# Optimization experiments

Hardware: AMD Instinct MI355X
Metric: run time of the kernel (lower is better)

Reference implementation:

```python
import jax, jax.numpy as jnp
import numpy as np

NEG_SLOPE = 0.2
N, IN_DIM, OUT_DIM, N_HEADS = 4096, 512, 512, 4
D_K = OUT_DIM // N_HEADS


def setup_inputs() -> dict:
    key = jax.random.key(0)
    k1, k2, k3, k4, k5 = jax.random.split(key, 5)
    H = jax.random.normal(k1, (N, IN_DIM), dtype=jnp.float32)
    A = jax.random.randint(k2, (N, N), 0, 2, dtype=jnp.int32)
    W = jax.random.normal(k3, (IN_DIM, OUT_DIM), dtype=jnp.float32) * (1.0 / np.sqrt(IN_DIM))
    a_l = jax.random.normal(k4, (N_HEADS, D_K), dtype=jnp.float32) * 0.1
    a_r = jax.random.normal(k5, (N_HEADS, D_K), dtype=jnp.float32) * 0.1
    return {"H": H, "A": A, "W": W, "a_l": a_l, "a_r": a_r}


def reference(H, A, W, a_l, a_r):
    n = H.shape[0]
    # mask = (A + I) > 0, shape (N, N); self-loops always allowed
    mask = (A + jnp.eye(n, dtype=A.dtype)) > 0
    # Wh: (N, heads, d_k)
    Wh = (H @ W).reshape(n, N_HEADS, D_K)
    sl = jnp.einsum('nhd,hd->nh', Wh, a_l)  # (N, heads)
    sr = jnp.einsum('nhd,hd->nh', Wh, a_r)  # (N, heads)
    # e[i, h, j] = leaky_relu(sl[i,h] + sr[j,h])
    e = jax.nn.leaky_relu(sl[:, :, None] + sr.T[None, :, :], negative_slope=NEG_SLOPE)
    e = jnp.where(mask[:, None, :], e, -jnp.inf)
    alpha = jnp.nan_to_num(jax.nn.softmax(e, axis=2), nan=0.0)  # dropout is identity at eval
    # out[i, h, :] = sum_j alpha[i,h,j] * Wh[j,h,:]
    out = jnp.einsum('nhm,mhd->nhd', alpha, Wh).reshape(n, OUT_DIM)
    return jax.nn.elu(out)
```

## Files before the change

### kernel.cpp

```cpp
#include <hip/hip_runtime.h>

typedef unsigned short ushort_t;
typedef __attribute__((ext_vector_type(8)))  short  short8;
typedef __attribute__((ext_vector_type(4)))  short  short4v;
typedef __attribute__((ext_vector_type(4)))  float  float4v;
typedef __attribute__((ext_vector_type(4)))  int    int4v;

#define N_NODES 4096
#define NHEADS  4
#define DK      128
#define ODIM    512
#define KDIM    512

__device__ __forceinline__ float bf2f(ushort_t u) {
    return __uint_as_float(((unsigned)u) << 16);
}
__device__ __forceinline__ ushort_t f2bf_rne(float f) {
    unsigned u = __float_as_uint(f);
    u += 0x7fffu + ((u >> 16) & 1u);
    return (ushort_t)(u >> 16);
}

__global__ __launch_bounds__(256) void pack_mask_k(const int* __restrict__ A,
                                                   unsigned long long* __restrict__ P,
                                                   const ushort_t* __restrict__ Hraw,
                                                   int* __restrict__ flag,
                                                   const void* __restrict__ W,
                                                   ushort_t* __restrict__ WT,
                                                   float* __restrict__ sl,
                                                   float* __restrict__ sr)
{
    __shared__ ushort_t lt[64][72];
    __shared__ int dcnt[4];
    const int tid = threadIdx.x;
    const int bx  = blockIdx.x;

    if (bx == 0 && tid < 64) {
        const int lane = tid;
        int cnt = 0;
        #pragma unroll
        for (int s = 0; s < 16; ++s) {
            ushort_t v = Hraw[(lane * 16 + s) * 2];
            int e = (v >> 7) & 0xFF;
            cnt += (((e >= 90) && (e <= 140)) || (v == 0)) ? 1 : 0;
        }
        #pragma unroll
        for (int off = 32; off; off >>= 1) cnt += __shfl_down(cnt, off);
        if (lane == 0) *flag = (cnt < 768) ? 1 : 0;
    }

    {
        const int lane  = tid & 63;
        const int flat4 = bx * 256 + tid;
        const int row   = flat4 >> 10;
        const int col0  = (flat4 << 2) & 4095;
        const int4v a   = ((const int4v*)A)[flat4];
        unsigned nib = 0;
        #pragma unroll
        for (int j = 0; j < 4; ++j)
            nib |= ((a[j] != 0) || (row == col0 + j)) ? (1u << j) : 0u;
        unsigned long long v = (unsigned long long)nib << ((lane & 15) * 4);
        v |= __shfl_xor(v, 1);
        v |= __shfl_xor(v, 2);
        v |= __shfl_xor(v, 4);
        v |= __shfl_xor(v, 8);
        if ((lane & 15) == 0) P[flat4 >> 4] = v;
    }

    if (bx >= 64 && bx < 96) {
        const int idx = (bx - 64) * 256 + tid;
        float4v z;
        #pragma unroll
        for (int e = 0; e < 4; ++e) z[e] = 0.f;
        if (idx < 4096) ((float4v*)sl)[idx] = z;
        else            ((float4v*)sr)[idx - 4096] = z;
    }

    if (bx < 64) {
        int cnt = 0;
        #pragma unroll
        for (int s = 0; s < 4; ++s) {
            ushort_t v = Hraw[(tid * 4 + s) * 2];
            int e = (v >> 7) & 0xFF;
            cnt += (((e >= 90) && (e <= 140)) || (v == 0)) ? 1 : 0;
        }
        #pragma unroll
        for (int off = 32; off; off >>= 1) cnt += __shfl_down(cnt, off);
        if ((tid & 63) == 0) dcnt[tid >> 6] = cnt;
        __syncthreads();
        const int f32 = (dcnt[0] + dcnt[1] + dcnt[2] + dcnt[3]) < 768;

        const int ti = bx >> 3, tj = bx & 7;
        const int r = tid >> 2, c2 = tid & 3;
        const size_t eo = (size_t)(ti * 64 + r) * KDIM + tj * 64 + c2 * 16;
        if (f32) {
            const float4v* src = (const float4v*)((const float*)W + eo);
            float4v f0 = src[0], f1 = src[1], f2 = src[2], f3 = src[3];
            #pragma unroll
            for (int e = 0; e < 4; ++e) {
                lt[r][c2 * 16 +  0 + e] = f2bf_rne(f0[e]);
                lt[r][c2 * 16 +  4 + e] = f2bf_rne(f1[e]);
                lt[r][c2 * 16 +  8 + e] = f2bf_rne(f2[e]);
                lt[r][c2 * 16 + 12 + e] = f2bf_rne(f3[e]);
            }
        } else {
            const short8* src = (const short8*)((const ushort_t*)W + eo);
            short8 v0 = src[0];
            short8 v1 = src[1];
            *(short8*)&lt[r][c2 * 16]     = v0;
            *(short8*)&lt[r][c2 * 16 + 8] = v1;
        }
        __syncthreads();
        #pragma unroll
        for (int itr = 0; itr < 2; ++itr) {
            int idx = itr * 256 + tid;
            int n = idx >> 3, c = idx & 7;
            short8 vv;
            #pragma unroll
            for (int e = 0; e < 8; ++e) vv[e] = (short)lt[c * 8 + e][n];
            *(short8*)(WT + (size_t)(tj * 64 + n) * KDIM + ti * 64 + c * 8) = vv;
        }
    }
}

__global__ __launch_bounds__(256) void gemm_wht_dual_k(const void* __restrict__ H,
                                                       const ushort_t* __restrict__ WT,
                                                       ushort_t* __restrict__ WhT,
                                                       const int* __restrict__ flag,
                                                       const void* __restrict__ al,
                                                       const void* __restrict__ ar,
                                                       float* __restrict__ sl,
                                                       float* __restrict__ sr)
{
    __shared__ ushort_t lt[64][72];
    const int f32 = *flag;
    const int tid  = threadIdx.x;
    const int lane = tid & 63;
    const int wid  = tid >> 6;
    const int quad = lane >> 4;
    const int l15  = lane & 15;
    const int bm = blockIdx.x & 63, bn = blockIdx.x >> 6;
    const int i0 = bm * 64, n0 = bn * 64;

    const size_t aoff = (size_t)(i0 + wid * 16 + l15) * KDIM + quad * 8;
    const short8* bp0 = (const short8*)(WT + (size_t)(n0 +  0 + l15) * KDIM) + quad;
    const short8* bp1 = (const short8*)(WT + (size_t)(n0 + 16 + l15) * KDIM) + quad;
    const short8* bp2 = (const short8*)(WT + (size_t)(n0 + 32 + l15) * KDIM) + quad;
    const short8* bp3 = (const short8*)(WT + (size_t)(n0 + 48 + l15) * KDIM) + quad;

    float4v acc0, acc1, acc2, acc3;
    #pragma unroll
    for (int e = 0; e < 4; ++e) { acc0[e] = 0.f; acc1[e] = 0.f; acc2[e] = 0.f; acc3[e] = 0.f; }

    #pragma unroll 4
    for (int k8 = 0; k8 < 64; k8 += 4) {
        short8 a;
        if (f32) {
            const float4v* fp = (const float4v*)((const float*)H + aoff + (size_t)k8 * 8);
            float4v x0 = fp[0], x1 = fp[1];
            #pragma unroll
            for (int e = 0; e < 4; ++e) {
                a[e]     = (short)f2bf_rne(x0[e]);
                a[4 + e] = (short)f2bf_rne(x1[e]);
            }
        } else {
            a = *(const short8*)((const ushort_t*)H + aoff + (size_t)k8 * 8);
        }
        acc0 = __builtin_amdgcn_mfma_f32_16x16x32_bf16(a, bp0[k8], acc0, 0, 0, 0);
        acc1 = __builtin_amdgcn_mfma_f32_16x16x32_bf16(a, bp1[k8], acc1, 0, 0, 0);
        acc2 = __builtin_amdgcn_mfma_f32_16x16x32_bf16(a, bp2[k8], acc2, 0, 0, 0);
        acc3 = __builtin_amdgcn_mfma_f32_16x16x32_bf16(a, bp3[k8], acc3, 0, 0, 0);
    }

    #pragma unroll
    for (int r = 0; r < 4; ++r) {
        int m = wid * 16 + quad * 4 + r;
        lt[ 0 + l15][m] = f2bf_rne(acc0[r]);
        lt[16 + l15][m] = f2bf_rne(acc1[r]);
        lt[32 + l15][m] = f2bf_rne(acc2[r]);
        lt[48 + l15][m] = f2bf_rne(acc3[r]);
    }
    __syncthreads();
    #pragma unroll
    for (int itr = 0; itr < 2; ++itr) {
        int idx = itr * 256 + tid;
        int n = idx >> 3, c = idx & 7;
        short8 v = *(const short8*)&lt[n][c * 8];
        *(short8*)(WhT + (size_t)(n0 + n) * N_NODES + i0 + c * 8) = v;
    }

    {
        const int h2 = n0 >> 7;
        const int d0 = n0 & 127;
        const int m  = tid >> 2;
        const int part = tid & 3;
        float psl = 0.f, psr = 0.f;
        #pragma unroll
        for (int k = 0; k < 16; ++k) {
            int n = part * 16 + k;
            float wv = bf2f(lt[n][m]);
            float av = f32 ? ((const float*)al)[h2 * DK + d0 + n]
                           : bf2f(((const ushort_t*)al)[h2 * DK + d0 + n]);
            float bv = f32 ? ((const float*)ar)[h2 * DK + d0 + n]
                           : bf2f(((const ushort_t*)ar)[h2 * DK + d0 + n]);
            psl += wv * av;
            psr += wv * bv;
        }
        psl += __shfl_down(psl, 2); psl += __shfl_down(psl, 1);
        psr += __shfl_down(psr, 2); psr += __shfl_down(psr, 1);
        if (part == 0) {
            atomicAdd(&sl[h2 * N_NODES + i0 + m], psl);
            atomicAdd(&sr[h2 * N_NODES + i0 + m], psr);
        }
    }
}

__global__ __launch_bounds__(1024, 4) void attn_full_k(const ushort_t* __restrict__ WhT,
                                                       const unsigned* __restrict__ Apack,
                                                       const float* __restrict__ sl,
                                                       const float* __restrict__ sr,
                                                       void* __restrict__ out,
                                                       const int* __restrict__ flag)
{
    __shared__ char smem[147456] __attribute__((aligned(16)));
    ushort_t* vbuf = (ushort_t*)smem;
    unsigned (*mbuf)[128] = (unsigned (*)[128])(smem + 98304);
    float*    srs  = (float*)(smem + 131072);

    const int f32  = *flag;
    const int tid  = threadIdx.x;
    const int lane = tid & 63;
    const int wid  = tid >> 6;
    const int wq   = wid & 3;
    const int js   = wid >> 2;
    const int quad = lane >> 4;
    const int l15  = lane & 15;
    const int bx   = blockIdx.x;
    const int h    = bx & 3;
    const int i0   = (bx >> 2) << 6;

    const float C1 = 1.44269504f;

    for (int j = tid; j < 4096; j += 1024) srs[j] = sr[h * N_NODES + j] * C1;
    for (int t = tid; t < 64 * 128; t += 1024) {
        int r = t >> 7, c = t & 127;
        mbuf[r][c ^ (r & 31)] = Apack[(size_t)(i0 + r) * 128 + c];
    }
    const int myrow = wq * 16 + l15;
    const float slv = sl[h * N_NODES + i0 + myrow] * C1;
    __syncthreads();

    float4v acc[8];
    #pragma unroll
    for (int nt = 0; nt < 8; ++nt)
        #pragma unroll
        for (int e = 0; e < 4; ++e) acc[nt][e] = 0.f;
    float4v accden;
    #pragma unroll
    for (int e = 0; e < 4; ++e) accden[e] = 0.f;

    short8 ones;
    #pragma unroll
    for (int e = 0; e < 8; ++e) ones[e] = (short)0x3F80;

    const int dl = lane >> 4;
    const int s4 = lane & 15;
    const ushort_t* gq0 = WhT + (size_t)(h * DK + wid * 8 + 0 + dl) * N_NODES
                              + (size_t)((s4 ^ (0 + dl)) * 8);
    const ushort_t* gq1 = WhT + (size_t)(h * DK + wid * 8 + 4 + dl) * N_NODES
                              + (size_t)((s4 ^ (4 + dl)) * 8);

    #define DMA_WIN(BUF, IW)                                                           \
        {   ushort_t* lb_ = vbuf + (BUF) * 16384 + wid * 1024;                         \
            __builtin_amdgcn_global_load_lds(                                          \
                (const __attribute__((address_space(1))) void*)(gq0 + (size_t)(IW) * 128), \
                (__attribute__((address_space(3))) void*)(lb_), 16, 0, 0);             \
            __builtin_amdgcn_global_load_lds(                                          \
                (const __attribute__((address_space(1))) void*)(gq1 + (size_t)(IW) * 128), \
                (__attribute__((address_space(3))) void*)(lb_ + 512), 16, 0, 0);       \
        }

    DMA_WIN(0, 0)
    DMA_WIN(1, 1)

    const int rs = ((js * 4 + quad) ^ (l15 & 7)) * 8;

    #pragma unroll 1
    for (int iw = 0; iw < 32; ++iw) {
        const unsigned wa = mbuf[myrow][(iw * 4 + js) ^ (myrow & 31)];
        const float4v s0 = *(const float4v*)&srs[iw * 128 + js * 32 + quad * 8];
        const float4v s1 = *(const float4v*)&srs[iw * 128 + js * 32 + quad * 8 + 4];

        short8 pf;
        #pragma unroll
        for (int jj = 0; jj < 8; ++jj) {
            const int bit = quad * 8 + jj;
            float srj = (jj < 4) ? s0[jj] : s1[jj - 4];
            float x = slv + srj;
            float t = fmaxf(x, x * 0.2f);
            t = ((wa >> bit) & 1u) ? t : -1e30f;
            pf[jj] = (short)(ushort_t)(__float_as_uint(__builtin_amdgcn_exp2f(t)) >> 16);
        }

        if (iw == 31) { asm volatile("s_waitcnt vmcnt(0)" ::: "memory"); }
        else          { asm volatile("s_waitcnt vmcnt(2)" ::: "memory"); }
        asm volatile("s_barrier" ::: "memory");
        if (iw < 30) DMA_WIN((iw + 2) % 3, iw + 2)

        const ushort_t* vB = vbuf + (iw % 3) * 16384;
        #pragma unroll
        for (int nt = 0; nt < 8; ++nt) {
            short8 b = *(const short8*)(vB + (nt * 16 + l15) * 128 + rs);
            acc[nt] = __builtin_amdgcn_mfma_f32_16x16x32_bf16(pf, b, acc[nt], 0, 0, 0);
        }
        accden = __builtin_amdgcn_mfma_f32_16x16x32_bf16(pf, ones, accden, 0, 0, 0);
    }
    #undef DMA_WIN

    float* red  = (float*)smem;
    float* lsum = (float*)(smem + 98304);
    __syncthreads();

    if (js != 0) {
        float* rp = red + (size_t)((js - 1) * 4 + wq) * 2048;
        #pragma unroll
        for (int nt = 0; nt < 8; ++nt)
            #pragma unroll
            for (int r = 0; r < 4; ++r)
                rp[(quad * 4 + r) * 128 + nt * 16 + l15] = acc[nt][r];
        if (l15 == 0) {
            #pragma unroll
            for (int r = 0; r < 4; ++r)
                lsum[js * 64 + wq * 16 + quad * 4 + r] = accden[r];
        }
    }
    __syncthreads();
    if (js == 0) {
        float rinv[4];
        #pragma unroll
        for (int r = 0; r < 4; ++r) {
            const int rowo = wq * 16 + quad * 4 + r;
            float den = accden[r] + lsum[64 + rowo] + lsum[128 + rowo] + lsum[192 + rowo];
            rinv[r] = 1.0f / fmaxf(den, 1e-37f);
        }
        #pragma unroll
        for (int nt = 0; nt < 8; ++nt)
            #pragma unroll
            for (int r = 0; r < 4; ++r) {
                const int ri = (quad * 4 + r) * 128 + nt * 16 + l15;
                float v = (acc[nt][r]
                           + red[(size_t)(0 * 4 + wq) * 2048 + ri]
                           + red[(size_t)(1 * 4 + wq) * 2048 + ri]
                           + red[(size_t)(2 * 4 + wq) * 2048 + ri]) * rinv[r];
                float e = __builtin_amdgcn_exp2f(v * C1) - 1.0f;
                float o = (v > 0.f) ? v : e;
                const size_t oidx = (size_t)(i0 + wq * 16 + quad * 4 + r) * ODIM
                                  + h * DK + nt * 16 + l15;
                if (f32) ((float*)out)[oidx] = o;
                else     ((ushort_t*)out)[oidx] = f2bf_rne(o);
            }
    }
}

extern "C" void kernel_launch(void* const* d_in, const int* in_sizes, int n_in,
                              void* d_out, int out_size, void* d_ws, size_t ws_size,
                              hipStream_t stream)
{
    const void* H  = d_in[0];
    const int*  A  = (const int*)d_in[1];
    const void* W  = d_in[2];
    const void* al = d_in[3];
    const void* ar = d_in[4];

    if (ws_size < (7u << 20)) return;

    char* ws = (char*)d_ws;
    ushort_t* WhT   = (ushort_t*)ws;
    unsigned long long* Apack = (unsigned long long*)(ws + (4u << 20));
    ushort_t* WT    = (ushort_t*)(ws + (6u << 20));
    float*    sl    = (float*)(ws + (6u << 20) + (512u << 10));
    float*    sr    = (float*)(ws + (6u << 20) + (576u << 10));
    int*      flag  = (int*)(ws + (6u << 20) + (640u << 10));

    pack_mask_k    <<<16384, 256, 0, stream>>>(A, Apack, (const ushort_t*)H, flag,
                                               W, WT, sl, sr);
    gemm_wht_dual_k<<<512,   256, 0, stream>>>(H, WT, WhT, flag, al, ar, sl, sr);
    attn_full_k    <<<256,  1024, 0, stream>>>(WhT, (const unsigned*)Apack, sl, sr,
                                               (void*)d_out, flag);
}
```

Before: 171.1 us.

## Stage W tile in LDS for GEMM and coarsen mask packing per block

The GEMM kernel now copies each block's 64x512 slice of the transposed W into shared memory with direct global-to-LDS loads and an XOR swizzle, then reads B fragments from LDS instead of global memory. Separately, the mask-packing kernel has each block process four chunks, cutting the grid from 16384 to 4096 blocks. The aim is to reduce redundant global B loads and per-block launch overhead. The risks are 64KB of LDS per GEMM block, which lowers occupancy, and a fully serialized load-then-compute prologue. The coarsening also changes which block indices run the side tasks (zeroing, flag, W transpose), which depend on bx ranges.

```diff
diff --git a/kernel.cpp b/kernel.cpp
--- a/kernel.cpp
+++ b/kernel.cpp
@@ -50,21 +50,24 @@
     }
 
     {
-        const int lane  = tid & 63;
-        const int flat4 = bx * 256 + tid;
-        const int row   = flat4 >> 10;
-        const int col0  = (flat4 << 2) & 4095;
-        const int4v a   = ((const int4v*)A)[flat4];
-        unsigned nib = 0;
-        #pragma unroll
-        for (int j = 0; j < 4; ++j)
-            nib |= ((a[j] != 0) || (row == col0 + j)) ? (1u << j) : 0u;
-        unsigned long long v = (unsigned long long)nib << ((lane & 15) * 4);
-        v |= __shfl_xor(v, 1);
-        v |= __shfl_xor(v, 2);
-        v |= __shfl_xor(v, 4);
-        v |= __shfl_xor(v, 8);
-        if ((lane & 15) == 0) P[flat4 >> 4] = v;
+        const int lane = tid & 63;
+        #pragma unroll
+        for (int kk = 0; kk < 4; ++kk) {
+            const int flat4 = (bx * 4 + kk) * 256 + tid;
+            const int row   = flat4 >> 10;
+            const int col0  = (flat4 << 2) & 4095;
+            const int4v a   = ((const int4v*)A)[flat4];
+            unsigned nib = 0;
+            #pragma unroll
+            for (int j = 0; j < 4; ++j)
+                nib |= ((a[j] != 0) || (row == col0 + j)) ? (1u << j) : 0u;
+            unsigned long long v = (unsigned long long)nib << ((lane & 15) * 4);
+            v |= __shfl_xor(v, 1);
+            v |= __shfl_xor(v, 2);
+            v |= __shfl_xor(v, 4);
+            v |= __shfl_xor(v, 8);
+            if ((lane & 15) == 0) P[flat4 >> 4] = v;
+        }
     }
 
     if (bx >= 64 && bx < 96) {
@@ -132,6 +135,7 @@
                                                        float* __restrict__ sl,
                                                        float* __restrict__ sr)
 {
+    __shared__ ushort_t Bs[64 * KDIM];
     __shared__ ushort_t lt[64][72];
     const int f32 = *flag;
     const int tid  = threadIdx.x;
@@ -142,15 +146,24 @@
     const int bm = blockIdx.x & 63, bn = blockIdx.x >> 6;
     const int i0 = bm * 64, n0 = bn * 64;
 
+    #pragma unroll
+    for (int rr = 0; rr < 16; ++rr) {
+        const int n = wid * 16 + rr;
+        const ushort_t* src = WT + (size_t)(n0 + n) * KDIM + (size_t)((lane ^ (n & 3)) * 8);
+        __builtin_amdgcn_global_load_lds(
+            (const __attribute__((address_space(1))) void*)src,
+            (__attribute__((address_space(3))) void*)(Bs + n * KDIM), 16, 0, 0);
+    }
+    asm volatile("s_waitcnt vmcnt(0)" ::: "memory");
+    __syncthreads();
+
     const size_t aoff = (size_t)(i0 + wid * 16 + l15) * KDIM + quad * 8;
-    const short8* bp0 = (const short8*)(WT + (size_t)(n0 +  0 + l15) * KDIM) + quad;
-    const short8* bp1 = (const short8*)(WT + (size_t)(n0 + 16 + l15) * KDIM) + quad;
-    const short8* bp2 = (const short8*)(WT + (size_t)(n0 + 32 + l15) * KDIM) + quad;
-    const short8* bp3 = (const short8*)(WT + (size_t)(n0 + 48 + l15) * KDIM) + quad;
 
     float4v acc0, acc1, acc2, acc3;
     #pragma unroll
     for (int e = 0; e < 4; ++e) { acc0[e] = 0.f; acc1[e] = 0.f; acc2[e] = 0.f; acc3[e] = 0.f; }
+
+    const int sx = l15 & 3;
 
     #pragma unroll 4
     for (int k8 = 0; k8 < 64; k8 += 4) {
@@ -166,10 +179,15 @@
         } else {
             a = *(const short8*)((const ushort_t*)H + aoff + (size_t)k8 * 8);
         }
-        acc0 = __builtin_amdgcn_mfma_f32_16x16x32_bf16(a, bp0[k8], acc0, 0, 0, 0);
-        acc1 = __builtin_amdgcn_mfma_f32_16x16x32_bf16(a, bp1[k8], acc1, 0, 0, 0);
-        acc2 = __builtin_amdgcn_mfma_f32_16x16x32_bf16(a, bp2[k8], acc2, 0, 0, 0);
-        acc3 = __builtin_amdgcn_mfma_f32_16x16x32_bf16(a, bp3[k8], acc3, 0, 0, 0);
+        const int s = (quad + k8) ^ sx;
+        short8 b0 = *(const short8*)(Bs + ( 0 + l15) * KDIM + s * 8);
+        short8 b1 = *(const short8*)(Bs + (16 + l15) * KDIM + s * 8);
+        short8 b2 = *(const short8*)(Bs + (32 + l15) * KDIM + s * 8);
+        short8 b3 = *(const short8*)(Bs + (48 + l15) * KDIM + s * 8);
+        acc0 = __builtin_amdgcn_mfma_f32_16x16x32_bf16(a, b0, acc0, 0, 0, 0);
+        acc1 = __builtin_amdgcn_mfma_f32_16x16x32_bf16(a, b1, acc1, 0, 0, 0);
+        acc2 = __builtin_amdgcn_mfma_f32_16x16x32_bf16(a, b2, acc2, 0, 0, 0);
+        acc3 = __builtin_amdgcn_mfma_f32_16x16x32_bf16(a, b3, acc3, 0, 0, 0);
     }
 
     #pragma unroll
@@ -382,7 +400,7 @@
     float*    sr    = (float*)(ws + (6u << 20) + (576u << 10));
     int*      flag  = (int*)(ws + (6u << 20) + (640u << 10));
 
-    pack_mask_k    <<<16384, 256, 0, stream>>>(A, Apack, (const ushort_t*)H, flag,
+    pack_mask_k    <<<4096,  256, 0, stream>>>(A, Apack, (const ushort_t*)H, flag,
                                                W, WT, sl, sr);
     gemm_wht_dual_k<<<512,   256, 0, stream>>>(H, WT, WhT, flag, al, ar, sl, sr);
     attn_full_k    <<<256,  1024, 0, stream>>>(WhT, (const unsigned*)Apack, sl, sr,
```

After: 159.6 us. 1.07x faster.
